# Kernel optimization log

Hardware: AMD Instinct MI355X
Metric: run time of the kernel (lower is better)

## Reference

```python
import jax, jax.numpy as jnp
from jax import lax
import numpy as np


def _lstm_layer(x, W_ih, W_hh, b_ih, b_hh):
    # x: (T, B, in_dim); gate order i, f, g, o (PyTorch convention)
    T, B, _ = x.shape
    H = W_hh.shape[1]
    # precompute input projections for all timesteps (one big GEMM)
    x_proj = jnp.einsum('tbi,gi->tbg', x, W_ih) + b_ih + b_hh  # (T, B, 4H)

    def step(carry, xt):
        h, c = carry
        gates = xt + h @ W_hh.T  # (B, 4H)
        i, f, g, o = jnp.split(gates, 4, axis=-1)
        c = jax.nn.sigmoid(f) * c + jax.nn.sigmoid(i) * jnp.tanh(g)
        h = jax.nn.sigmoid(o) * jnp.tanh(c)
        return (h, c), h

    h0 = jnp.zeros((B, H), dtype=x.dtype)
    c0 = jnp.zeros((B, H), dtype=x.dtype)
    (hT, cT), hs = lax.scan(step, (h0, c0), x_proj)
    return hs, hT, cT


def setup_inputs() -> dict:
    key = jax.random.key(0)
    ks = jax.random.split(key, 12)
    T, B, D_in, H, D_out = 1024, 64, 256, 512, 256
    s_in = 1.0 / np.sqrt(H)
    inp = {
        'x': jax.random.normal(ks[0], (T, B, D_in), jnp.float32),
        'W_ih0': jax.random.uniform(ks[1], (4 * H, D_in), jnp.float32, -s_in, s_in),
        'W_hh0': jax.random.uniform(ks[2], (4 * H, H), jnp.float32, -s_in, s_in),
        'b_ih0': jax.random.uniform(ks[3], (4 * H,), jnp.float32, -s_in, s_in),
        'b_hh0': jax.random.uniform(ks[4], (4 * H,), jnp.float32, -s_in, s_in),
        'W_ih1': jax.random.uniform(ks[5], (4 * H, H), jnp.float32, -s_in, s_in),
        'W_hh1': jax.random.uniform(ks[6], (4 * H, H), jnp.float32, -s_in, s_in),
        'b_ih1': jax.random.uniform(ks[7], (4 * H,), jnp.float32, -s_in, s_in),
        'b_hh1': jax.random.uniform(ks[8], (4 * H,), jnp.float32, -s_in, s_in),
        'W_out': jax.random.uniform(ks[9], (D_out, H), jnp.float32, -s_in, s_in),
        'b_out': jax.random.uniform(ks[10], (D_out,), jnp.float32, -s_in, s_in),
    }
    return inp


def reference(x, W_ih0, W_hh0, b_ih0, b_hh0, W_ih1, W_hh1, b_ih1, b_hh1, W_out, b_out):
    h1s, h1, c1 = _lstm_layer(x, W_ih0, W_hh0, b_ih0, b_hh0)
    h2s, h2, c2 = _lstm_layer(h1s, W_ih1, W_hh1, b_ih1, b_hh1)
    out = jnp.einsum('tbh,oh->tbo', h2s, W_out) + b_out  # (T, B, D_out)
    hn = jnp.stack([h1, h2], axis=0)  # (num_layers, B, H)
    cn = jnp.stack([c1, c2], axis=0)
    return (out, hn, cn)
```

## Files before the change

kernel.cpp:

```cpp
#include <hip/hip_runtime.h>

#define TT   1024
#define BB   64
#define DIN  256
#define HH   512
#define DOUT 256

#define NWG_L0  64
#define NWG_L1  128
#define NWG_OUT 8
#define NWG_TOT 200

typedef short bf16x8 __attribute__((ext_vector_type(8)));
typedef float f32x4  __attribute__((ext_vector_type(4)));
typedef unsigned u32x4 __attribute__((ext_vector_type(4)));

__device__ bf16x8 g_xf[TT * 2048];
__device__ bf16x8 g_h1f[8][4096];
__device__ bf16x8 g_h2f[8][4096];
__device__ bf16x8 g_h1z[4096];
__device__ bf16x8 g_h2z[4096];

__device__ unsigned g_flg[520 * 16];
__device__ unsigned g_iter;

__device__ __forceinline__ unsigned* FLG(int idx) { return &g_flg[idx * 16]; }

__device__ __forceinline__ u32x4 ldg_cv16(const void* p) {
    u32x4 r;
    asm volatile("global_load_dwordx4 %0, %1, off sc0 sc1"
                 : "=&v"(r) : "v"(p) : "memory");
    return r;
}
__device__ __forceinline__ void stg_cv16(void* p, u32x4 v) {
    asm volatile("global_store_dwordx4 %0, %1, off sc0 sc1" :: "v"(p), "v"(v) : "memory");
}
__device__ __forceinline__ void stg_cv_u32(void* p, unsigned v) {
    asm volatile("global_store_dword %0, %1, off sc0 sc1" :: "v"(p), "v"(v) : "memory");
}
__device__ __forceinline__ void wait_vm0(void) {
    asm volatile("s_waitcnt vmcnt(0)" ::: "memory");
}

__device__ __forceinline__ void waitpoll(const unsigned* p, unsigned tgt, int active, int tid) {
    for (;;) {
        unsigned v = 0xFFFFFFFFu;
        if (active)
            asm volatile("global_load_dword %0, %1, off sc0 sc1\n\t"
                         "s_waitcnt vmcnt(0)"
                         : "=&v"(v) : "v"(p) : "memory");
        if (__all(v >= tgt)) break;
        __builtin_amdgcn_s_sleep(1);
    }
    __syncthreads();
}

__device__ __forceinline__ float sigf(float v) { return 1.f / (1.f + __expf(-v)); }
__device__ __forceinline__ float tanh_fast(float v) { return 2.f / (1.f + __expf(-2.f * v)) - 1.f; }

__device__ __forceinline__ short f2bf(float f) {
    unsigned u = __builtin_bit_cast(unsigned, f);
    unsigned r = (u + 0x7FFFu + ((u >> 16) & 1u)) >> 16;
    return (short)r;
}

__device__ __forceinline__ bf16x8 pack8(float4 v0, float4 v1) {
    bf16x8 r;
    r[0] = f2bf(v0.x); r[1] = f2bf(v0.y); r[2] = f2bf(v0.z); r[3] = f2bf(v0.w);
    r[4] = f2bf(v1.x); r[5] = f2bf(v1.y); r[6] = f2bf(v1.z); r[7] = f2bf(v1.w);
    return r;
}

extern "C" __global__ void __launch_bounds__(256)
pack_x(const float* __restrict__ x) {
    const int t = blockIdx.x, tid = threadIdx.x;
    const float* xt = x + (size_t)t * BB * DIN;
    bf16x8* dst = g_xf + (size_t)t * 2048;
    #pragma unroll
    for (int u = 0; u < 8; ++u) {
        const int f = u * 256 + tid;
        const int lane_ = f & 63, ctks = f >> 6;
        const int ct = ctks & 3, ks = ctks >> 2;
        const int b  = ct * 16 + (lane_ & 15);
        const int kb = ks * 32 + (lane_ >> 4) * 8;
        const float4* s = (const float4*)(xt + b * DIN + kb);
        dst[f] = pack8(s[0], s[1]);
    }
}

__device__ void run_l0(int lwg, int tid,
                       const float* __restrict__ wih, const float* __restrict__ whh,
                       const float* __restrict__ bih, const float* __restrict__ bhh,
                       float* __restrict__ out, unsigned Q, bf16x8* sB, short* sH)
{
    constexpr int NCT = 2, NKSA = DIN / 32, NKS = NKSA + HH / 32;
    constexpr int NST = NKS * NCT / 4;
    constexpr int NCXR = NKSA * NCT / 4;

    const int lane = tid & 63, lo = lane & 15, hi = lane >> 4;
    const int w = tid >> 6;
    const int grp = lwg & 1, ub = lwg >> 1;
    const int ctbase = grp * 2;
    const int wv = ub * 4 + w, jbase = wv * 4;
    const int grow = (lo & 3) * HH + jbase + (lo >> 2);

    bf16x8 aF[NKS];
    #pragma unroll
    for (int ks = 0; ks < NKS; ++ks) {
        const float* wr = (ks < NKSA) ? wih + (size_t)grow * DIN + ks * 32 + hi * 8
                                      : whh + (size_t)grow * HH + (ks - NKSA) * 32 + hi * 8;
        const float4* p = (const float4*)wr;
        aF[ks] = pack8(p[0], p[1]);
    }
    f32x4 biasv;
    #pragma unroll
    for (int r = 0; r < 4; ++r)
        biasv[r] = bih[r * HH + jbase + hi] + bhh[r * HH + jbase + hi];

    const unsigned Qb = Q * 2048u;
    float cst[NCT] = {0.f, 0.f};

    for (int t = 0; t < TT; ++t) {
        {
            const unsigned* wp = g_flg; unsigned wt = 0; int wa = 0;
            const int bp = (t >= 8) && ((t & 3) == 0);
            if (w == 0) { if (lane < 32 && t >= 1) { wp = FLG(0 + grp * 32 + lane);
                                                     wt = Qb + t; wa = 1; } }
            else if (w == 1) { if (bp) {
                wp = FLG(192 + (grp * 2 + (lane >> 5)) * 32 + (lane & 31));
                wt = Qb + t - 4; wa = 1; } }
            else if (w == 2) { if (bp && lane < 32) {
                wp = FLG(320 + grp * 32 + lane); wt = Qb + t - 4; wa = 1; } }
            waitpoll(wp, wt, wa, tid);
        }

        const bf16x8* srcA = g_xf + (size_t)t * 2048;
        const bf16x8* srcB = (t == 0) ? g_h1z : g_h1f[(t - 1) & 7];

        u32x4 stg[NST];
        #pragma unroll
        for (int r = 0; r < NST; ++r) {
            const int ri = r * 4 + w, ks = ri / NCT, c = ri % NCT;
            if (r < NCXR) stg[r] = *(const u32x4*)&srcA[(ks * 4 + ctbase + c) * 64 + lane];
            else          stg[r] = ldg_cv16(&srcB[((ks - NKSA) * 4 + ctbase + c) * 64 + lane]);
        }
        wait_vm0();
        #pragma unroll
        for (int r = 0; r < NST; ++r)
            ((u32x4*)sB)[(r * 4 + w) * 64 + lane] = stg[r];
        __syncthreads();
        if (tid == 0) stg_cv_u32(FLG(320 + grp * 32 + ub), Qb + t);

        f32x4 acc[NCT] = {biasv, biasv};
        #pragma unroll
        for (int ks = 0; ks < NKS; ++ks)
            #pragma unroll
            for (int c = 0; c < NCT; ++c)
                acc[c] = __builtin_amdgcn_mfma_f32_16x16x32_bf16(
                    aF[ks], sB[(ks * NCT + c) * 64 + lane], acc[c], 0, 0, 0);

        #pragma unroll
        for (int c = 0; c < NCT; ++c) {
            const float gi = acc[c][0], gf = acc[c][1];
            const float gg = acc[c][2], go = acc[c][3];
            const float cn_ = sigf(gf) * cst[c] + sigf(gi) * tanh_fast(gg);
            const float hv  = sigf(go) * tanh_fast(cn_);
            cst[c] = cn_;
            sH[((c * 2 + (w >> 1)) * 16 + lo) * 8 + (w & 1) * 4 + hi] = f2bf(hv);
            if (t == TT - 1) {
                const int j = jbase + hi, b = (ctbase + c) * 16 + lo;
                const size_t base = (size_t)TT * BB * DOUT;
                out[base + (size_t)b * HH + j] = hv;
                out[base + (size_t)2 * BB * HH + (size_t)b * HH + j] = cn_;
            }
        }
        __syncthreads();

        u32x4* ringW = (u32x4*)g_h1f[t & 7];
        if (tid < 64) {
            const int c = tid >> 5, r = tid & 31, hi2 = r >> 4, lo2 = r & 15;
            const int f = ((ub >> 1) * 4 + ctbase + c) * 64 + ((ub & 1) * 2 + hi2) * 16 + lo2;
            stg_cv16(ringW + f, *(const u32x4*)&sH[((c * 2 + hi2) * 16 + lo2) * 8]);
        }
        wait_vm0();
        if (tid == 0) stg_cv_u32(FLG(0 + grp * 32 + ub), Qb + t + 1);
    }
}

__device__ void run_l1(int lwg, int tid,
                       const float* __restrict__ wih, const float* __restrict__ whh,
                       const float* __restrict__ bih, const float* __restrict__ bhh,
                       float* __restrict__ out, unsigned Q, bf16x8* sB, short* sH)
{
    constexpr int NKSA = HH / 32, NKS = 2 * NKSA;
    constexpr int NSTA = NKSA / 4, NSTB = NKSA / 4;

    const int lane = tid & 63, lo = lane & 15, hi = lane >> 4;
    const int w = tid >> 6;
    const int grp = lwg & 3, ub = lwg >> 2;
    const int ctbase = grp;
    const int wv = ub * 4 + w, jbase = wv * 4;
    const int grow = (lo & 3) * HH + jbase + (lo >> 2);

    bf16x8 aF[NKS];
    #pragma unroll
    for (int ks = 0; ks < NKS; ++ks) {
        const float* wr = (ks < NKSA) ? wih + (size_t)grow * HH + ks * 32 + hi * 8
                                      : whh + (size_t)grow * HH + (ks - NKSA) * 32 + hi * 8;
        const float4* p = (const float4*)wr;
        aF[ks] = pack8(p[0], p[1]);
    }
    f32x4 biasv;
    #pragma unroll
    for (int r = 0; r < 4; ++r)
        biasv[r] = bih[r * HH + jbase + hi] + bhh[r * HH + jbase + hi];

    const unsigned Qb = Q * 2048u;
    float cst = 0.f;

    {
        const unsigned* wp = g_flg; unsigned wt = 0; int wa = 0;
        if (w == 0 && lane < 32) { wp = FLG(0 + (grp >> 1) * 32 + lane); wt = Qb + 1; wa = 1; }
        waitpoll(wp, wt, wa, tid);
    }

    for (int t = 0; t < TT; ++t) {
        const bf16x8* srcA = g_h1f[t & 7];
        const bf16x8* srcB = (t == 0) ? g_h2z : g_h2f[(t - 1) & 7];

        u32x4 stgA[NSTA];
        #pragma unroll
        for (int r = 0; r < NSTA; ++r) {
            const int ks = r * 4 + w;
            stgA[r] = ldg_cv16(&srcA[(ks * 4 + ctbase) * 64 + lane]);
        }
        wait_vm0();
        #pragma unroll
        for (int r = 0; r < NSTA; ++r)
            ((u32x4*)sB)[(r * 4 + w) * 64 + lane] = stgA[r];
        __syncthreads();
        if (tid == 0) stg_cv_u32(FLG(192 + grp * 32 + ub), Qb + t + 1);

        {
            const unsigned* wp = g_flg; unsigned wt = 0; int wa = 0;
            if (w == 0 && lane < 32 && t >= 1) { wp = FLG(64 + grp * 32 + lane);
                                                 wt = Qb + t; wa = 1; }
            waitpoll(wp, wt, wa, tid);
        }

        u32x4 stgB[NSTB];
        #pragma unroll
        for (int r = 0; r < NSTB; ++r) {
            const int ks = r * 4 + w;
            stgB[r] = ldg_cv16(&srcB[(ks * 4 + ctbase) * 64 + lane]);
        }
        f32x4 acc = biasv;
        #pragma unroll
        for (int ks = 0; ks < NKSA; ++ks)
            acc = __builtin_amdgcn_mfma_f32_16x16x32_bf16(
                aF[ks], sB[ks * 64 + lane], acc, 0, 0, 0);
        wait_vm0();
        #pragma unroll
        for (int r = 0; r < NSTB; ++r)
            ((u32x4*)sB)[(NKSA + r * 4 + w) * 64 + lane] = stgB[r];
        __syncthreads();
        if (tid == 0) stg_cv_u32(FLG(384 + grp * 32 + ub), Qb + t);
        #pragma unroll
        for (int ks = NKSA; ks < NKS; ++ks)
            acc = __builtin_amdgcn_mfma_f32_16x16x32_bf16(
                aF[ks], sB[ks * 64 + lane], acc, 0, 0, 0);

        {
            const float gi = acc[0], gf = acc[1], gg = acc[2], go = acc[3];
            const float cn_ = sigf(gf) * cst + sigf(gi) * tanh_fast(gg);
            const float hv  = sigf(go) * tanh_fast(cn_);
            cst = cn_;
            sH[((w >> 1) * 16 + lo) * 8 + (w & 1) * 4 + hi] = f2bf(hv);
            if (t == TT - 1) {
                const int j = jbase + hi, b = ctbase * 16 + lo;
                const size_t base = (size_t)TT * BB * DOUT;
                out[base + (size_t)BB * HH + (size_t)b * HH + j] = hv;
                out[base + (size_t)3 * BB * HH + (size_t)b * HH + j] = cn_;
            }
        }
        __syncthreads();

        u32x4* ringW = (u32x4*)g_h2f[t & 7];
        if (tid < 32) {
            const int hi2 = tid >> 4, lo2 = tid & 15;
            const int f = ((ub >> 1) * 4 + ctbase) * 64 + ((ub & 1) * 2 + hi2) * 16 + lo2;
            stg_cv16(ringW + f, *(const u32x4*)&sH[(hi2 * 16 + lo2) * 8]);
        }
        wait_vm0();
        if (tid == 0) stg_cv_u32(FLG(64 + grp * 32 + ub), Qb + t + 1);

        if (t < TT - 1) {
            const unsigned* wp = g_flg; unsigned wt = 0; int wa = 0;
            const int bp = (t >= 7) && ((t & 3) == 3);
            if (w == 0) { if (lane < 32) { wp = FLG(0 + (grp >> 1) * 32 + lane);
                                           wt = Qb + t + 2; wa = 1; } }
            else if (w == 1) { if (bp) {
                if (lane < 32)      { wp = FLG(384 + grp * 32 + lane);
                                      wt = Qb + t - 3; wa = 1; }
                else if (lane < 36) { wp = FLG(512 + (grp >> 1) * 4 + (lane - 32));
                                      wt = Qb + t - 3; wa = 1; } } }
            waitpoll(wp, wt, wa, tid);
        }
    }
}

__device__ void run_out(int lwg, int tid,
                        const float* __restrict__ wout, const float* __restrict__ bout,
                        float* __restrict__ out, unsigned Q, bf16x8* sB)
{
    constexpr int NKS = HH / 32;
    constexpr int NST = 8;
    const int lane = tid & 63, lo = lane & 15, hi = lane >> 4;
    const int w = tid >> 6;
    const int cp = lwg & 1, ob = lwg >> 1;
    const int ctbase = cp * 2;
    const int obase = (ob * 4 + w) * 16;
    const unsigned Qb = Q * 2048u;

    bf16x8 aF[NKS];
    #pragma unroll
    for (int ks = 0; ks < NKS; ++ks) {
        const float4* p = (const float4*)(wout + (size_t)(obase + lo) * HH + ks * 32 + hi * 8);
        aF[ks] = pack8(p[0], p[1]);
    }
    f32x4 biasv;
    #pragma unroll
    for (int r = 0; r < 4; ++r) biasv[r] = bout[obase + hi * 4 + r];

    for (int t = 0; t < TT; ++t) {
        const unsigned* wp = g_flg; unsigned wt = 0; int wa = 0;
        if (w == 0) {
            wp = FLG(64 + (ctbase + (lane >> 5)) * 32 + (lane & 31));
            wt = Qb + t + 1; wa = 1;
        }
        waitpoll(wp, wt, wa, tid);

        const bf16x8* src = g_h2f[t & 7];
        u32x4 stg[NST];
        #pragma unroll
        for (int r = 0; r < NST; ++r) {
            const int ri = r * 4 + w;
            const int ks = ri >> 1, c = ri & 1;
            stg[r] = ldg_cv16(&src[(ks * 4 + ctbase + c) * 64 + lane]);
        }
        wait_vm0();
        #pragma unroll
        for (int r = 0; r < NST; ++r)
            ((u32x4*)sB)[(r * 4 + w) * 64 + lane] = stg[r];
        __syncthreads();
        if (tid == 0) stg_cv_u32(FLG(512 + cp * 4 + ob), Qb + t + 1);

        f32x4 acc[2] = {biasv, biasv};
        #pragma unroll
        for (int ks = 0; ks < NKS; ++ks)
            #pragma unroll
            for (int c = 0; c < 2; ++c)
                acc[c] = __builtin_amdgcn_mfma_f32_16x16x32_bf16(
                    aF[ks], sB[(ks * 2 + c) * 64 + lane], acc[c], 0, 0, 0);
        #pragma unroll
        for (int c = 0; c < 2; ++c)
            #pragma unroll
            for (int r = 0; r < 4; ++r) {
                const int b = (ctbase + c) * 16 + lo, o = obase + hi * 4 + r;
                out[(size_t)t * BB * DOUT + (size_t)b * DOUT + o] = acc[c][r];
            }
    }
}

extern "C" __global__ void __launch_bounds__(256, 1)
lstm2_fused(const float* __restrict__ x,
            const float* __restrict__ wih0, const float* __restrict__ whh0,
            const float* __restrict__ bih0, const float* __restrict__ bhh0,
            const float* __restrict__ wih1, const float* __restrict__ whh1,
            const float* __restrict__ bih1, const float* __restrict__ bhh1,
            const float* __restrict__ wout, const float* __restrict__ bout,
            float* __restrict__ out)
{
    __shared__ bf16x8 sB[3072];
    __shared__ __align__(16) short sH[2 * 2 * 16 * 8];

    const int tid = threadIdx.x, wg = blockIdx.x;
    const unsigned Q = __hip_atomic_load(&g_iter, __ATOMIC_RELAXED, __HIP_MEMORY_SCOPE_AGENT);

    if (wg < NWG_L0)
        run_l0(wg, tid, wih0, whh0, bih0, bhh0, out, Q, sB, sH);
    else if (wg < NWG_L0 + NWG_L1)
        run_l1(wg - NWG_L0, tid, wih1, whh1, bih1, bhh1, out, Q, sB, sH);
    else
        run_out(wg - NWG_L0 - NWG_L1, tid, wout, bout, out, Q, sB);

    if (wg == 0 && tid == 0)
        __hip_atomic_store(&g_iter, Q + 1, __ATOMIC_RELAXED, __HIP_MEMORY_SCOPE_AGENT);
}

extern "C" void kernel_launch(void* const* d_in, const int* in_sizes, int n_in,
                              void* d_out, int out_size, void* d_ws, size_t ws_size,
                              hipStream_t stream) {
    const float* x    = (const float*)d_in[0];
    const float* wih0 = (const float*)d_in[1];
    const float* whh0 = (const float*)d_in[2];
    const float* bih0 = (const float*)d_in[3];
    const float* bhh0 = (const float*)d_in[4];
    const float* wih1 = (const float*)d_in[5];
    const float* whh1 = (const float*)d_in[6];
    const float* bih1 = (const float*)d_in[7];
    const float* bhh1 = (const float*)d_in[8];
    const float* wout = (const float*)d_in[9];
    const float* bout = (const float*)d_in[10];
    float* out = (float*)d_out;

    hipLaunchKernelGGL(pack_x, dim3(TT), dim3(256), 0, stream, x);
    hipLaunchKernelGGL(lstm2_fused, dim3(NWG_TOT), dim3(256), 0, stream,
                       x, wih0, whh0, bih0, bhh0, wih1, whh1, bih1, bhh1,
                       wout, bout, out);
}
```

Measured before the change: 3.730 ms.

## Replace flag-based h-ring handoff with per-element tagged data polling

Hidden-state ring buffers now store each bf16 value together with a 16-bit iteration tag in a 32-bit word. Consumers poll the data itself until every tag matches, so producer-side flag stores, the LDS staging/sync before publishing, and separate readiness-flag waits are removed. This aims to shorten the per-timestep critical path of the recurrent dependency chain. In exchange it doubles the bytes moved per handoff and adds tag checks and repeated reloads while spinning.

Measured after the change: 5.194 ms. 1.39x slower.

```diff
diff --git a/kernel.cpp b/kernel.cpp
--- a/kernel.cpp
+++ b/kernel.cpp
@@ -16,10 +16,10 @@
 typedef unsigned u32x4 __attribute__((ext_vector_type(4)));
 
 __device__ bf16x8 g_xf[TT * 2048];
-__device__ bf16x8 g_h1f[8][4096];
-__device__ bf16x8 g_h2f[8][4096];
-__device__ bf16x8 g_h1z[4096];
-__device__ bf16x8 g_h2z[4096];
+
+#define SLOT_U32 (4 * 16 * 512)
+__device__ unsigned g_h1t[8][SLOT_U32];
+__device__ unsigned g_h2t[8][SLOT_U32];
 
 __device__ unsigned g_flg[520 * 16];
 __device__ unsigned g_iter;
@@ -31,9 +31,6 @@
     asm volatile("global_load_dwordx4 %0, %1, off sc0 sc1"
                  : "=&v"(r) : "v"(p) : "memory");
     return r;
-}
-__device__ __forceinline__ void stg_cv16(void* p, u32x4 v) {
-    asm volatile("global_store_dwordx4 %0, %1, off sc0 sc1" :: "v"(p), "v"(v) : "memory");
 }
 __device__ __forceinline__ void stg_cv_u32(void* p, unsigned v) {
     asm volatile("global_store_dword %0, %1, off sc0 sc1" :: "v"(p), "v"(v) : "memory");
@@ -55,6 +52,21 @@
     __syncthreads();
 }
 
+__device__ __forceinline__ int tagok(u32x4 a, u32x4 b, unsigned etag) {
+    return (int)((a[0] & 0xFFFFu) == etag) & (int)((a[1] & 0xFFFFu) == etag)
+         & (int)((a[2] & 0xFFFFu) == etag) & (int)((a[3] & 0xFFFFu) == etag)
+         & (int)((b[0] & 0xFFFFu) == etag) & (int)((b[1] & 0xFFFFu) == etag)
+         & (int)((b[2] & 0xFFFFu) == etag) & (int)((b[3] & 0xFFFFu) == etag);
+}
+__device__ __forceinline__ u32x4 untag(u32x4 a, u32x4 b) {
+    u32x4 p;
+    p[0] = (a[0] >> 16) | (a[1] & 0xFFFF0000u);
+    p[1] = (a[2] >> 16) | (a[3] & 0xFFFF0000u);
+    p[2] = (b[0] >> 16) | (b[1] & 0xFFFF0000u);
+    p[3] = (b[2] >> 16) | (b[3] & 0xFFFF0000u);
+    return p;
+}
+
 __device__ __forceinline__ float sigf(float v) { return 1.f / (1.f + __expf(-v)); }
 __device__ __forceinline__ float tanh_fast(float v) { return 2.f / (1.f + __expf(-2.f * v)) - 1.f; }
 
@@ -69,6 +81,10 @@
     r[0] = f2bf(v0.x); r[1] = f2bf(v0.y); r[2] = f2bf(v0.z); r[3] = f2bf(v0.w);
     r[4] = f2bf(v1.x); r[5] = f2bf(v1.y); r[6] = f2bf(v1.z); r[7] = f2bf(v1.w);
     return r;
+}
+
+__device__ __forceinline__ int pidx_of(int j, int b) {
+    return ((j >> 5) * 4 + (b >> 4)) * 512 + (((j >> 3) & 3) * 16 + (b & 15)) * 8 + (j & 7);
 }
 
 extern "C" __global__ void __launch_bounds__(256)
@@ -91,17 +107,14 @@
 __device__ void run_l0(int lwg, int tid,
                        const float* __restrict__ wih, const float* __restrict__ whh,
                        const float* __restrict__ bih, const float* __restrict__ bhh,
-                       float* __restrict__ out, unsigned Q, bf16x8* sB, short* sH)
+                       float* __restrict__ out, unsigned Q, bf16x8* sB)
 {
-    constexpr int NCT = 2, NKSA = DIN / 32, NKS = NKSA + HH / 32;
-    constexpr int NST = NKS * NCT / 4;
-    constexpr int NCXR = NKSA * NCT / 4;
-
+    constexpr int NKSA = 8, NKS = 24;
     const int lane = tid & 63, lo = lane & 15, hi = lane >> 4;
     const int w = tid >> 6;
     const int grp = lwg & 1, ub = lwg >> 1;
     const int ctbase = grp * 2;
-    const int wv = ub * 4 + w, jbase = wv * 4;
+    const int jbase = (ub * 4 + w) * 4;
     const int grow = (lo & 3) * HH + jbase + (lo >> 2);
 
     bf16x8 aF[NKS];
@@ -118,88 +131,102 @@
         biasv[r] = bih[r * HH + jbase + hi] + bhh[r * HH + jbase + hi];
 
     const unsigned Qb = Q * 2048u;
-    float cst[NCT] = {0.f, 0.f};
+    float cst[2] = {0.f, 0.f};
 
     for (int t = 0; t < TT; ++t) {
-        {
-            const unsigned* wp = g_flg; unsigned wt = 0; int wa = 0;
-            const int bp = (t >= 8) && ((t & 3) == 0);
-            if (w == 0) { if (lane < 32 && t >= 1) { wp = FLG(0 + grp * 32 + lane);
-                                                     wt = Qb + t; wa = 1; } }
-            else if (w == 1) { if (bp) {
-                wp = FLG(192 + (grp * 2 + (lane >> 5)) * 32 + (lane & 31));
-                wt = Qb + t - 4; wa = 1; } }
-            else if (w == 2) { if (bp && lane < 32) {
-                wp = FLG(320 + grp * 32 + lane); wt = Qb + t - 4; wa = 1; } }
-            waitpoll(wp, wt, wa, tid);
-        }
-
-        const bf16x8* srcA = g_xf + (size_t)t * 2048;
-        const bf16x8* srcB = (t == 0) ? g_h1z : g_h1f[(t - 1) & 7];
-
-        u32x4 stg[NST];
-        #pragma unroll
-        for (int r = 0; r < NST; ++r) {
-            const int ri = r * 4 + w, ks = ri / NCT, c = ri % NCT;
-            if (r < NCXR) stg[r] = *(const u32x4*)&srcA[(ks * 4 + ctbase + c) * 64 + lane];
-            else          stg[r] = ldg_cv16(&srcB[((ks - NKSA) * 4 + ctbase + c) * 64 + lane]);
-        }
-        wait_vm0();
-        #pragma unroll
-        for (int r = 0; r < NST; ++r)
-            ((u32x4*)sB)[(r * 4 + w) * 64 + lane] = stg[r];
+        __syncthreads();
+
+        u32x4 sa[4];
+        #pragma unroll
+        for (int r = 0; r < 4; ++r) {
+            const int ri = r * 4 + w, ks = ri >> 1, c = ri & 1;
+            sa[r] = *(const u32x4*)&g_xf[(size_t)t * 2048 + (ks * 4 + ctbase + c) * 64 + lane];
+        }
+        #pragma unroll
+        for (int r = 0; r < 4; ++r)
+            ((u32x4*)sB)[(r * 4 + w) * 64 + lane] = sa[r];
+
+        if (t > 0) {
+            const unsigned etag = (Qb + t) & 0xFFFFu;
+            const unsigned* slot = g_h1t[(t - 1) & 7];
+            u32x4 da[8], db[8];
+            for (;;) {
+                #pragma unroll
+                for (int r = 0; r < 8; ++r) {
+                    const int ri = r * 4 + w, ks = ri >> 1, c = ri & 1;
+                    const unsigned* p = slot + (ks * 4 + ctbase + c) * 512 + lane * 8;
+                    da[r] = ldg_cv16(p); db[r] = ldg_cv16(p + 4);
+                }
+                wait_vm0();
+                int ok = 1;
+                #pragma unroll
+                for (int r = 0; r < 8; ++r) ok &= tagok(da[r], db[r], etag);
+                if (__all(ok)) break;
+                __builtin_amdgcn_s_sleep(1);
+            }
+            #pragma unroll
+            for (int r = 0; r < 8; ++r)
+                ((u32x4*)sB)[(16 + r * 4 + w) * 64 + lane] = untag(da[r], db[r]);
+        }
         __syncthreads();
         if (tid == 0) stg_cv_u32(FLG(320 + grp * 32 + ub), Qb + t);
 
-        f32x4 acc[NCT] = {biasv, biasv};
-        #pragma unroll
-        for (int ks = 0; ks < NKS; ++ks)
-            #pragma unroll
-            for (int c = 0; c < NCT; ++c)
+        if (((t & 3) == 0) && t >= 8) {
+            const unsigned* wp = g_flg; unsigned wt = 0; int wa = 0;
+            if (w == 1) { wp = FLG(192 + (2 * grp + (lane >> 5)) * 32 + (lane & 31));
+                          wt = Qb + t - 4; wa = 1; }
+            else if (w == 2 && lane < 32) { wp = FLG(320 + grp * 32 + lane);
+                                            wt = Qb + t - 4; wa = 1; }
+            waitpoll(wp, wt, wa, tid);
+        }
+
+        f32x4 acc[2] = {biasv, biasv};
+        #pragma unroll
+        for (int ks = 0; ks < NKSA; ++ks)
+            #pragma unroll
+            for (int c = 0; c < 2; ++c)
                 acc[c] = __builtin_amdgcn_mfma_f32_16x16x32_bf16(
-                    aF[ks], sB[(ks * NCT + c) * 64 + lane], acc[c], 0, 0, 0);
-
-        #pragma unroll
-        for (int c = 0; c < NCT; ++c) {
+                    aF[ks], sB[(ks * 2 + c) * 64 + lane], acc[c], 0, 0, 0);
+        if (t > 0) {
+            #pragma unroll
+            for (int ks = NKSA; ks < NKS; ++ks)
+                #pragma unroll
+                for (int c = 0; c < 2; ++c)
+                    acc[c] = __builtin_amdgcn_mfma_f32_16x16x32_bf16(
+                        aF[ks], sB[(ks * 2 + c) * 64 + lane], acc[c], 0, 0, 0);
+        }
+
+        const unsigned ptag = (Qb + t + 1) & 0xFFFFu;
+        unsigned* slotW = g_h1t[t & 7];
+        #pragma unroll
+        for (int c = 0; c < 2; ++c) {
             const float gi = acc[c][0], gf = acc[c][1];
             const float gg = acc[c][2], go = acc[c][3];
             const float cn_ = sigf(gf) * cst[c] + sigf(gi) * tanh_fast(gg);
             const float hv  = sigf(go) * tanh_fast(cn_);
             cst[c] = cn_;
-            sH[((c * 2 + (w >> 1)) * 16 + lo) * 8 + (w & 1) * 4 + hi] = f2bf(hv);
+            const int j = jbase + hi, b = (ctbase + c) * 16 + lo;
+            stg_cv_u32(slotW + pidx_of(j, b),
+                       ((unsigned)(unsigned short)f2bf(hv) << 16) | ptag);
             if (t == TT - 1) {
-                const int j = jbase + hi, b = (ctbase + c) * 16 + lo;
                 const size_t base = (size_t)TT * BB * DOUT;
                 out[base + (size_t)b * HH + j] = hv;
                 out[base + (size_t)2 * BB * HH + (size_t)b * HH + j] = cn_;
             }
         }
-        __syncthreads();
-
-        u32x4* ringW = (u32x4*)g_h1f[t & 7];
-        if (tid < 64) {
-            const int c = tid >> 5, r = tid & 31, hi2 = r >> 4, lo2 = r & 15;
-            const int f = ((ub >> 1) * 4 + ctbase + c) * 64 + ((ub & 1) * 2 + hi2) * 16 + lo2;
-            stg_cv16(ringW + f, *(const u32x4*)&sH[((c * 2 + hi2) * 16 + lo2) * 8]);
-        }
-        wait_vm0();
-        if (tid == 0) stg_cv_u32(FLG(0 + grp * 32 + ub), Qb + t + 1);
     }
 }
 
 __device__ void run_l1(int lwg, int tid,
                        const float* __restrict__ wih, const float* __restrict__ whh,
                        const float* __restrict__ bih, const float* __restrict__ bhh,
-                       float* __restrict__ out, unsigned Q, bf16x8* sB, short* sH)
+                       float* __restrict__ out, unsigned Q, bf16x8* sB)
 {
-    constexpr int NKSA = HH / 32, NKS = 2 * NKSA;
-    constexpr int NSTA = NKSA / 4, NSTB = NKSA / 4;
-
+    constexpr int NKSA = 16, NKS = 32;
     const int lane = tid & 63, lo = lane & 15, hi = lane >> 4;
     const int w = tid >> 6;
     const int grp = lwg & 3, ub = lwg >> 2;
-    const int ctbase = grp;
-    const int wv = ub * 4 + w, jbase = wv * 4;
+    const int jbase = (ub * 4 + w) * 4;
     const int grow = (lo & 3) * HH + jbase + (lo >> 2);
 
     bf16x8 aF[NKS];
@@ -218,93 +245,98 @@
     const unsigned Qb = Q * 2048u;
     float cst = 0.f;
 
-    {
-        const unsigned* wp = g_flg; unsigned wt = 0; int wa = 0;
-        if (w == 0 && lane < 32) { wp = FLG(0 + (grp >> 1) * 32 + lane); wt = Qb + 1; wa = 1; }
-        waitpoll(wp, wt, wa, tid);
-    }
-
     for (int t = 0; t < TT; ++t) {
-        const bf16x8* srcA = g_h1f[t & 7];
-        const bf16x8* srcB = (t == 0) ? g_h2z : g_h2f[(t - 1) & 7];
-
-        u32x4 stgA[NSTA];
-        #pragma unroll
-        for (int r = 0; r < NSTA; ++r) {
-            const int ks = r * 4 + w;
-            stgA[r] = ldg_cv16(&srcA[(ks * 4 + ctbase) * 64 + lane]);
-        }
-        wait_vm0();
-        #pragma unroll
-        for (int r = 0; r < NSTA; ++r)
-            ((u32x4*)sB)[(r * 4 + w) * 64 + lane] = stgA[r];
+        {
+            const unsigned etag = (Qb + t + 1) & 0xFFFFu;
+            const unsigned* slot = g_h1t[t & 7];
+            u32x4 da[4], db[4];
+            for (;;) {
+                #pragma unroll
+                for (int r = 0; r < 4; ++r) {
+                    const unsigned* p = slot + ((r * 4 + w) * 4 + grp) * 512 + lane * 8;
+                    da[r] = ldg_cv16(p); db[r] = ldg_cv16(p + 4);
+                }
+                wait_vm0();
+                int ok = 1;
+                #pragma unroll
+                for (int r = 0; r < 4; ++r) ok &= tagok(da[r], db[r], etag);
+                if (__all(ok)) break;
+                __builtin_amdgcn_s_sleep(1);
+            }
+            #pragma unroll
+            for (int r = 0; r < 4; ++r)
+                ((u32x4*)sB)[(r * 4 + w) * 64 + lane] = untag(da[r], db[r]);
+        }
         __syncthreads();
         if (tid == 0) stg_cv_u32(FLG(192 + grp * 32 + ub), Qb + t + 1);
 
-        {
+        f32x4 acc = biasv;
+        if (t > 0) {
+            const unsigned etag = (Qb + t) & 0xFFFFu;
+            const unsigned* slot = g_h2t[(t - 1) & 7];
+            u32x4 da[4], db[4];
+            #pragma unroll
+            for (int r = 0; r < 4; ++r) {
+                const unsigned* p = slot + ((r * 4 + w) * 4 + grp) * 512 + lane * 8;
+                da[r] = ldg_cv16(p); db[r] = ldg_cv16(p + 4);
+            }
+            #pragma unroll
+            for (int ks = 0; ks < NKSA; ++ks)
+                acc = __builtin_amdgcn_mfma_f32_16x16x32_bf16(
+                    aF[ks], sB[ks * 64 + lane], acc, 0, 0, 0);
+            for (;;) {
+                wait_vm0();
+                int ok = 1;
+                #pragma unroll
+                for (int r = 0; r < 4; ++r) ok &= tagok(da[r], db[r], etag);
+                if (__all(ok)) break;
+                __builtin_amdgcn_s_sleep(1);
+                #pragma unroll
+                for (int r = 0; r < 4; ++r) {
+                    const unsigned* p = slot + ((r * 4 + w) * 4 + grp) * 512 + lane * 8;
+                    da[r] = ldg_cv16(p); db[r] = ldg_cv16(p + 4);
+                }
+            }
+            #pragma unroll
+            for (int r = 0; r < 4; ++r)
+                ((u32x4*)sB)[(16 + r * 4 + w) * 64 + lane] = untag(da[r], db[r]);
+            __syncthreads();
+            if (tid == 0) stg_cv_u32(FLG(384 + grp * 32 + ub), Qb + t);
+            #pragma unroll
+            for (int ks = NKSA; ks < NKS; ++ks)
+                acc = __builtin_amdgcn_mfma_f32_16x16x32_bf16(
+                    aF[ks], sB[ks * 64 + lane], acc, 0, 0, 0);
+        } else {
+            #pragma unroll
+            for (int ks = 0; ks < NKSA; ++ks)
+                acc = __builtin_amdgcn_mfma_f32_16x16x32_bf16(
+                    aF[ks], sB[ks * 64 + lane], acc, 0, 0, 0);
+            __syncthreads();
+            if (tid == 0) stg_cv_u32(FLG(384 + grp * 32 + ub), Qb);
+        }
+
+        if (((t & 3) == 0) && t >= 8) {
             const unsigned* wp = g_flg; unsigned wt = 0; int wa = 0;
-            if (w == 0 && lane < 32 && t >= 1) { wp = FLG(64 + grp * 32 + lane);
-                                                 wt = Qb + t; wa = 1; }
+            if (w == 1) {
+                if (lane < 32)      { wp = FLG(384 + grp * 32 + lane); wt = Qb + t - 4; wa = 1; }
+                else if (lane < 36) { wp = FLG(512 + (grp >> 1) * 4 + (lane - 32));
+                                      wt = Qb + t - 4; wa = 1; }
+            }
             waitpoll(wp, wt, wa, tid);
         }
 
-        u32x4 stgB[NSTB];
-        #pragma unroll
-        for (int r = 0; r < NSTB; ++r) {
-            const int ks = r * 4 + w;
-            stgB[r] = ldg_cv16(&srcB[(ks * 4 + ctbase) * 64 + lane]);
-        }
-        f32x4 acc = biasv;
-        #pragma unroll
-        for (int ks = 0; ks < NKSA; ++ks)
-            acc = __builtin_amdgcn_mfma_f32_16x16x32_bf16(
-                aF[ks], sB[ks * 64 + lane], acc, 0, 0, 0);
-        wait_vm0();
-        #pragma unroll
-        for (int r = 0; r < NSTB; ++r)
-            ((u32x4*)sB)[(NKSA + r * 4 + w) * 64 + lane] = stgB[r];
-        __syncthreads();
-        if (tid == 0) stg_cv_u32(FLG(384 + grp * 32 + ub), Qb + t);
-        #pragma unroll
-        for (int ks = NKSA; ks < NKS; ++ks)
-            acc = __builtin_amdgcn_mfma_f32_16x16x32_bf16(
-                aF[ks], sB[ks * 64 + lane], acc, 0, 0, 0);
-
-        {
-            const float gi = acc[0], gf = acc[1], gg = acc[2], go = acc[3];
-            const float cn_ = sigf(gf) * cst + sigf(gi) * tanh_fast(gg);
-            const float hv  = sigf(go) * tanh_fast(cn_);
-            cst = cn_;
-            sH[((w >> 1) * 16 + lo) * 8 + (w & 1) * 4 + hi] = f2bf(hv);
-            if (t == TT - 1) {
-                const int j = jbase + hi, b = ctbase * 16 + lo;
-                const size_t base = (size_t)TT * BB * DOUT;
-                out[base + (size_t)BB * HH + (size_t)b * HH + j] = hv;
-                out[base + (size_t)3 * BB * HH + (size_t)b * HH + j] = cn_;
-            }
-        }
-        __syncthreads();
-
-        u32x4* ringW = (u32x4*)g_h2f[t & 7];
-        if (tid < 32) {
-            const int hi2 = tid >> 4, lo2 = tid & 15;
-            const int f = ((ub >> 1) * 4 + ctbase) * 64 + ((ub & 1) * 2 + hi2) * 16 + lo2;
-            stg_cv16(ringW + f, *(const u32x4*)&sH[(hi2 * 16 + lo2) * 8]);
-        }
-        wait_vm0();
-        if (tid == 0) stg_cv_u32(FLG(64 + grp * 32 + ub), Qb + t + 1);
-
-        if (t < TT - 1) {
-            const unsigned* wp = g_flg; unsigned wt = 0; int wa = 0;
-            const int bp = (t >= 7) && ((t & 3) == 3);
-            if (w == 0) { if (lane < 32) { wp = FLG(0 + (grp >> 1) * 32 + lane);
-                                           wt = Qb + t + 2; wa = 1; } }
-            else if (w == 1) { if (bp) {
-                if (lane < 32)      { wp = FLG(384 + grp * 32 + lane);
-                                      wt = Qb + t - 3; wa = 1; }
-                else if (lane < 36) { wp = FLG(512 + (grp >> 1) * 4 + (lane - 32));
-                                      wt = Qb + t - 3; wa = 1; } } }
-            waitpoll(wp, wt, wa, tid);
+        const float gi = acc[0], gf = acc[1], gg = acc[2], go = acc[3];
+        const float cn_ = sigf(gf) * cst + sigf(gi) * tanh_fast(gg);
+        const float hv  = sigf(go) * tanh_fast(cn_);
+        cst = cn_;
+        const unsigned ptag = (Qb + t + 1) & 0xFFFFu;
+        const int j = jbase + hi, b = grp * 16 + lo;
+        stg_cv_u32(g_h2t[t & 7] + pidx_of(j, b),
+                   ((unsigned)(unsigned short)f2bf(hv) << 16) | ptag);
+        if (t == TT - 1) {
+            const size_t base = (size_t)TT * BB * DOUT;
+            out[base + (size_t)BB * HH + (size_t)b * HH + j] = hv;
+            out[base + (size_t)3 * BB * HH + (size_t)b * HH + j] = cn_;
         }
     }
 }
@@ -314,7 +346,6 @@
                         float* __restrict__ out, unsigned Q, bf16x8* sB)
 {
     constexpr int NKS = HH / 32;
-    constexpr int NST = 8;
     const int lane = tid & 63, lo = lane & 15, hi = lane >> 4;
     const int w = tid >> 6;
     const int cp = lwg & 1, ob = lwg >> 1;
@@ -333,25 +364,29 @@
     for (int r = 0; r < 4; ++r) biasv[r] = bout[obase + hi * 4 + r];
 
     for (int t = 0; t < TT; ++t) {
-        const unsigned* wp = g_flg; unsigned wt = 0; int wa = 0;
-        if (w == 0) {
-            wp = FLG(64 + (ctbase + (lane >> 5)) * 32 + (lane & 31));
-            wt = Qb + t + 1; wa = 1;
-        }
-        waitpoll(wp, wt, wa, tid);
-
-        const bf16x8* src = g_h2f[t & 7];
-        u32x4 stg[NST];
-        #pragma unroll
-        for (int r = 0; r < NST; ++r) {
-            const int ri = r * 4 + w;
-            const int ks = ri >> 1, c = ri & 1;
-            stg[r] = ldg_cv16(&src[(ks * 4 + ctbase + c) * 64 + lane]);
-        }
-        wait_vm0();
-        #pragma unroll
-        for (int r = 0; r < NST; ++r)
-            ((u32x4*)sB)[(r * 4 + w) * 64 + lane] = stg[r];
+        __syncthreads();
+        {
+            const unsigned etag = (Qb + t + 1) & 0xFFFFu;
+            const unsigned* slot = g_h2t[t & 7];
+            u32x4 da[8], db[8];
+            for (;;) {
+                #pragma unroll
+                for (int r = 0; r < 8; ++r) {
+                    const int ri = r * 4 + w, ks = ri >> 1, c = ri & 1;
+                    const unsigned* p = slot + (ks * 4 + ctbase + c) * 512 + lane * 8;
+                    da[r] = ldg_cv16(p); db[r] = ldg_cv16(p + 4);
+                }
+                wait_vm0();
+                int ok = 1;
+                #pragma unroll
+                for (int r = 0; r < 8; ++r) ok &= tagok(da[r], db[r], etag);
+                if (__all(ok)) break;
+                __builtin_amdgcn_s_sleep(1);
+            }
+            #pragma unroll
+            for (int r = 0; r < 8; ++r)
+                ((u32x4*)sB)[(r * 4 + w) * 64 + lane] = untag(da[r], db[r]);
+        }
         __syncthreads();
         if (tid == 0) stg_cv_u32(FLG(512 + cp * 4 + ob), Qb + t + 1);
 
@@ -382,15 +417,14 @@
             float* __restrict__ out)
 {
     __shared__ bf16x8 sB[3072];
-    __shared__ __align__(16) short sH[2 * 2 * 16 * 8];
 
     const int tid = threadIdx.x, wg = blockIdx.x;
     const unsigned Q = __hip_atomic_load(&g_iter, __ATOMIC_RELAXED, __HIP_MEMORY_SCOPE_AGENT);
 
     if (wg < NWG_L0)
-        run_l0(wg, tid, wih0, whh0, bih0, bhh0, out, Q, sB, sH);
+        run_l0(wg, tid, wih0, whh0, bih0, bhh0, out, Q, sB);
     else if (wg < NWG_L0 + NWG_L1)
-        run_l1(wg - NWG_L0, tid, wih1, whh1, bih1, bhh1, out, Q, sB, sH);
+        run_l1(wg - NWG_L0, tid, wih1, whh1, bih1, bhh1, out, Q, sB);
     else
         run_out(wg - NWG_L0 - NWG_L1, tid, wout, bout, out, Q, sB);
 
```

## Halve workgroup count with 8-wave workgroups to cut cross-WG flag polling

Applied to the files above, without the earlier changes.

Doubles the threads per workgroup to 512 (8 waves) and halves the number of workgroups per stage (layer0 32, layer1 64, output 4). Each workgroup now owns 32 hidden units instead of 16, so h-chunk ring writes and flag waits involve half as many producers. The change also drops the zero-initialised h buffers by skipping the recurrent MFMA at t=0, and restructures layer1 so all waits happen at the top of each step. The cost is more per-workgroup synchronisation over larger barriers and fewer CUs in use, which lowers parallelism per step.

Measured after the change: 3.996 ms. +7.1%, slower.

```diff
diff --git a/kernel.cpp b/kernel.cpp
--- a/kernel.cpp
+++ b/kernel.cpp
@@ -6,10 +6,10 @@
 #define HH   512
 #define DOUT 256
 
-#define NWG_L0  64
-#define NWG_L1  128
-#define NWG_OUT 8
-#define NWG_TOT 200
+#define NWG_L0  32
+#define NWG_L1  64
+#define NWG_OUT 4
+#define NWG_TOT 100
 
 typedef short bf16x8 __attribute__((ext_vector_type(8)));
 typedef float f32x4  __attribute__((ext_vector_type(4)));
@@ -18,10 +18,8 @@
 __device__ bf16x8 g_xf[TT * 2048];
 __device__ bf16x8 g_h1f[8][4096];
 __device__ bf16x8 g_h2f[8][4096];
-__device__ bf16x8 g_h1z[4096];
-__device__ bf16x8 g_h2z[4096];
-
-__device__ unsigned g_flg[520 * 16];
+
+__device__ unsigned g_flg[260 * 16];
 __device__ unsigned g_iter;
 
 __device__ __forceinline__ unsigned* FLG(int idx) { return &g_flg[idx * 16]; }
@@ -93,15 +91,12 @@
                        const float* __restrict__ bih, const float* __restrict__ bhh,
                        float* __restrict__ out, unsigned Q, bf16x8* sB, short* sH)
 {
-    constexpr int NCT = 2, NKSA = DIN / 32, NKS = NKSA + HH / 32;
-    constexpr int NST = NKS * NCT / 4;
-    constexpr int NCXR = NKSA * NCT / 4;
-
+    constexpr int NKSA = 8, NKS = 24;
     const int lane = tid & 63, lo = lane & 15, hi = lane >> 4;
     const int w = tid >> 6;
     const int grp = lwg & 1, ub = lwg >> 1;
     const int ctbase = grp * 2;
-    const int wv = ub * 4 + w, jbase = wv * 4;
+    const int jbase = ub * 32 + w * 4;
     const int grow = (lo & 3) * HH + jbase + (lo >> 2);
 
     bf16x8 aF[NKS];
@@ -118,55 +113,69 @@
         biasv[r] = bih[r * HH + jbase + hi] + bhh[r * HH + jbase + hi];
 
     const unsigned Qb = Q * 2048u;
-    float cst[NCT] = {0.f, 0.f};
+    float cst[2] = {0.f, 0.f};
 
     for (int t = 0; t < TT; ++t) {
         {
             const unsigned* wp = g_flg; unsigned wt = 0; int wa = 0;
             const int bp = (t >= 8) && ((t & 3) == 0);
-            if (w == 0) { if (lane < 32 && t >= 1) { wp = FLG(0 + grp * 32 + lane);
+            if (w == 0) { if (lane < 16 && t >= 1) { wp = FLG(0 + grp * 16 + lane);
                                                      wt = Qb + t; wa = 1; } }
-            else if (w == 1) { if (bp) {
-                wp = FLG(192 + (grp * 2 + (lane >> 5)) * 32 + (lane & 31));
-                wt = Qb + t - 4; wa = 1; } }
-            else if (w == 2) { if (bp && lane < 32) {
-                wp = FLG(320 + grp * 32 + lane); wt = Qb + t - 4; wa = 1; } }
+            else if (w == 1 && bp) {
+                if (lane < 32)      { wp = FLG(96 + (2 * grp + (lane >> 4)) * 16 + (lane & 15));
+                                      wt = Qb + t - 4; wa = 1; }
+                else if (lane < 48) { wp = FLG(160 + grp * 16 + (lane - 32));
+                                      wt = Qb + t - 4; wa = 1; }
+            }
             waitpoll(wp, wt, wa, tid);
         }
 
         const bf16x8* srcA = g_xf + (size_t)t * 2048;
-        const bf16x8* srcB = (t == 0) ? g_h1z : g_h1f[(t - 1) & 7];
-
-        u32x4 stg[NST];
-        #pragma unroll
-        for (int r = 0; r < NST; ++r) {
-            const int ri = r * 4 + w, ks = ri / NCT, c = ri % NCT;
-            if (r < NCXR) stg[r] = *(const u32x4*)&srcA[(ks * 4 + ctbase + c) * 64 + lane];
-            else          stg[r] = ldg_cv16(&srcB[((ks - NKSA) * 4 + ctbase + c) * 64 + lane]);
+        const bf16x8* srcB = g_h1f[(t - 1) & 7];
+        u32x4 stg[6];
+        #pragma unroll
+        for (int r = 0; r < 6; ++r) {
+            const int ri = r * 8 + w;
+            if (ri < 16) {
+                const int ks = ri >> 1, c = ri & 1;
+                stg[r] = *(const u32x4*)&srcA[(ks * 4 + ctbase + c) * 64 + lane];
+            } else if (t > 0) {
+                const int ks = (ri - 16) >> 1, c = (ri - 16) & 1;
+                stg[r] = ldg_cv16(&srcB[(ks * 4 + ctbase + c) * 64 + lane]);
+            }
         }
         wait_vm0();
         #pragma unroll
-        for (int r = 0; r < NST; ++r)
-            ((u32x4*)sB)[(r * 4 + w) * 64 + lane] = stg[r];
+        for (int r = 0; r < 6; ++r)
+            ((u32x4*)sB)[(r * 8 + w) * 64 + lane] = stg[r];
         __syncthreads();
-        if (tid == 0) stg_cv_u32(FLG(320 + grp * 32 + ub), Qb + t);
-
-        f32x4 acc[NCT] = {biasv, biasv};
-        #pragma unroll
-        for (int ks = 0; ks < NKS; ++ks)
-            #pragma unroll
-            for (int c = 0; c < NCT; ++c)
+        if (tid == 0) stg_cv_u32(FLG(160 + grp * 16 + ub), Qb + t);
+
+        f32x4 acc[2] = {biasv, biasv};
+        #pragma unroll
+        for (int ks = 0; ks < NKSA; ++ks)
+            #pragma unroll
+            for (int c = 0; c < 2; ++c)
                 acc[c] = __builtin_amdgcn_mfma_f32_16x16x32_bf16(
-                    aF[ks], sB[(ks * NCT + c) * 64 + lane], acc[c], 0, 0, 0);
-
-        #pragma unroll
-        for (int c = 0; c < NCT; ++c) {
+                    aF[ks], sB[(ks * 2 + c) * 64 + lane], acc[c], 0, 0, 0);
+        if (t > 0) {
+            #pragma unroll
+            for (int ks = NKSA; ks < NKS; ++ks)
+                #pragma unroll
+                for (int c = 0; c < 2; ++c)
+                    acc[c] = __builtin_amdgcn_mfma_f32_16x16x32_bf16(
+                        aF[ks], sB[(ks * 2 + c) * 64 + lane], acc[c], 0, 0, 0);
+        }
+
+        #pragma unroll
+        for (int c = 0; c < 2; ++c) {
             const float gi = acc[c][0], gf = acc[c][1];
             const float gg = acc[c][2], go = acc[c][3];
             const float cn_ = sigf(gf) * cst[c] + sigf(gi) * tanh_fast(gg);
             const float hv  = sigf(go) * tanh_fast(cn_);
             cst[c] = cn_;
-            sH[((c * 2 + (w >> 1)) * 16 + lo) * 8 + (w & 1) * 4 + hi] = f2bf(hv);
+            const int jp = w * 4 + hi;
+            sH[(c * 64 + (jp >> 3) * 16 + lo) * 8 + (jp & 7)] = f2bf(hv);
             if (t == TT - 1) {
                 const int j = jbase + hi, b = (ctbase + c) * 16 + lo;
                 const size_t base = (size_t)TT * BB * DOUT;
@@ -178,12 +187,13 @@
 
         u32x4* ringW = (u32x4*)g_h1f[t & 7];
         if (tid < 64) {
-            const int c = tid >> 5, r = tid & 31, hi2 = r >> 4, lo2 = r & 15;
-            const int f = ((ub >> 1) * 4 + ctbase + c) * 64 + ((ub & 1) * 2 + hi2) * 16 + lo2;
-            stg_cv16(ringW + f, *(const u32x4*)&sH[((c * 2 + hi2) * 16 + lo2) * 8]);
+            #pragma unroll
+            for (int c = 0; c < 2; ++c)
+                stg_cv16(ringW + (ub * 4 + ctbase + c) * 64 + tid,
+                         *(const u32x4*)&sH[(c * 64 + tid) * 8]);
         }
         wait_vm0();
-        if (tid == 0) stg_cv_u32(FLG(0 + grp * 32 + ub), Qb + t + 1);
+        if (tid == 0) stg_cv_u32(FLG(0 + grp * 16 + ub), Qb + t + 1);
     }
 }
 
@@ -192,14 +202,11 @@
                        const float* __restrict__ bih, const float* __restrict__ bhh,
                        float* __restrict__ out, unsigned Q, bf16x8* sB, short* sH)
 {
-    constexpr int NKSA = HH / 32, NKS = 2 * NKSA;
-    constexpr int NSTA = NKSA / 4, NSTB = NKSA / 4;
-
+    constexpr int NKSA = 16, NKS = 32;
     const int lane = tid & 63, lo = lane & 15, hi = lane >> 4;
     const int w = tid >> 6;
     const int grp = lwg & 3, ub = lwg >> 2;
-    const int ctbase = grp;
-    const int wv = ub * 4 + w, jbase = wv * 4;
+    const int jbase = ub * 32 + w * 4;
     const int grow = (lo & 3) * HH + jbase + (lo >> 2);
 
     bf16x8 aF[NKS];
@@ -218,66 +225,82 @@
     const unsigned Qb = Q * 2048u;
     float cst = 0.f;
 
-    {
-        const unsigned* wp = g_flg; unsigned wt = 0; int wa = 0;
-        if (w == 0 && lane < 32) { wp = FLG(0 + (grp >> 1) * 32 + lane); wt = Qb + 1; wa = 1; }
-        waitpoll(wp, wt, wa, tid);
-    }
-
     for (int t = 0; t < TT; ++t) {
-        const bf16x8* srcA = g_h1f[t & 7];
-        const bf16x8* srcB = (t == 0) ? g_h2z : g_h2f[(t - 1) & 7];
-
-        u32x4 stgA[NSTA];
-        #pragma unroll
-        for (int r = 0; r < NSTA; ++r) {
-            const int ks = r * 4 + w;
-            stgA[r] = ldg_cv16(&srcA[(ks * 4 + ctbase) * 64 + lane]);
-        }
-        wait_vm0();
-        #pragma unroll
-        for (int r = 0; r < NSTA; ++r)
-            ((u32x4*)sB)[(r * 4 + w) * 64 + lane] = stgA[r];
-        __syncthreads();
-        if (tid == 0) stg_cv_u32(FLG(192 + grp * 32 + ub), Qb + t + 1);
-
         {
             const unsigned* wp = g_flg; unsigned wt = 0; int wa = 0;
-            if (w == 0 && lane < 32 && t >= 1) { wp = FLG(64 + grp * 32 + lane);
+            const int bp = (t >= 8) && ((t & 3) == 0);
+            if (w == 0) { if (lane < 16) { wp = FLG(0 + (grp >> 1) * 16 + lane);
+                                           wt = Qb + t + 1; wa = 1; } }
+            else if (w == 1 && bp) {
+                if (lane < 16)      { wp = FLG(192 + grp * 16 + lane);
+                                      wt = Qb + t - 4; wa = 1; }
+                else if (lane < 18) { wp = FLG(256 + 2 * (grp >> 1) + (lane - 16));
+                                      wt = Qb + t - 4; wa = 1; }
+            }
+            waitpoll(wp, wt, wa, tid);
+        }
+
+        const bf16x8* srcA = g_h1f[t & 7];
+        u32x4 sa[2];
+        #pragma unroll
+        for (int r = 0; r < 2; ++r) {
+            const int ks = r * 8 + w;
+            sa[r] = ldg_cv16(&srcA[(ks * 4 + grp) * 64 + lane]);
+        }
+        wait_vm0();
+        #pragma unroll
+        for (int r = 0; r < 2; ++r)
+            ((u32x4*)sB)[(r * 8 + w) * 64 + lane] = sa[r];
+        __syncthreads();
+        if (tid == 0) stg_cv_u32(FLG(96 + grp * 16 + ub), Qb + t + 1);
+
+        {
+            const unsigned* wp = g_flg; unsigned wt = 0; int wa = 0;
+            if (w == 0 && lane < 16 && t >= 1) { wp = FLG(32 + grp * 16 + lane);
                                                  wt = Qb + t; wa = 1; }
             waitpoll(wp, wt, wa, tid);
         }
 
-        u32x4 stgB[NSTB];
-        #pragma unroll
-        for (int r = 0; r < NSTB; ++r) {
-            const int ks = r * 4 + w;
-            stgB[r] = ldg_cv16(&srcB[(ks * 4 + ctbase) * 64 + lane]);
-        }
         f32x4 acc = biasv;
-        #pragma unroll
-        for (int ks = 0; ks < NKSA; ++ks)
-            acc = __builtin_amdgcn_mfma_f32_16x16x32_bf16(
-                aF[ks], sB[ks * 64 + lane], acc, 0, 0, 0);
-        wait_vm0();
-        #pragma unroll
-        for (int r = 0; r < NSTB; ++r)
-            ((u32x4*)sB)[(NKSA + r * 4 + w) * 64 + lane] = stgB[r];
-        __syncthreads();
-        if (tid == 0) stg_cv_u32(FLG(384 + grp * 32 + ub), Qb + t);
-        #pragma unroll
-        for (int ks = NKSA; ks < NKS; ++ks)
-            acc = __builtin_amdgcn_mfma_f32_16x16x32_bf16(
-                aF[ks], sB[ks * 64 + lane], acc, 0, 0, 0);
+        if (t > 0) {
+            const bf16x8* srcB = g_h2f[(t - 1) & 7];
+            u32x4 sb[2];
+            #pragma unroll
+            for (int r = 0; r < 2; ++r) {
+                const int ks = r * 8 + w;
+                sb[r] = ldg_cv16(&srcB[(ks * 4 + grp) * 64 + lane]);
+            }
+            #pragma unroll
+            for (int ks = 0; ks < NKSA; ++ks)
+                acc = __builtin_amdgcn_mfma_f32_16x16x32_bf16(
+                    aF[ks], sB[ks * 64 + lane], acc, 0, 0, 0);
+            wait_vm0();
+            #pragma unroll
+            for (int r = 0; r < 2; ++r)
+                ((u32x4*)sB)[(16 + r * 8 + w) * 64 + lane] = sb[r];
+            __syncthreads();
+            if (tid == 0) stg_cv_u32(FLG(192 + grp * 16 + ub), Qb + t);
+            #pragma unroll
+            for (int ks = NKSA; ks < NKS; ++ks)
+                acc = __builtin_amdgcn_mfma_f32_16x16x32_bf16(
+                    aF[ks], sB[ks * 64 + lane], acc, 0, 0, 0);
+        } else {
+            #pragma unroll
+            for (int ks = 0; ks < NKSA; ++ks)
+                acc = __builtin_amdgcn_mfma_f32_16x16x32_bf16(
+                    aF[ks], sB[ks * 64 + lane], acc, 0, 0, 0);
+            if (tid == 0) stg_cv_u32(FLG(192 + grp * 16 + ub), Qb);
+        }
 
         {
             const float gi = acc[0], gf = acc[1], gg = acc[2], go = acc[3];
             const float cn_ = sigf(gf) * cst + sigf(gi) * tanh_fast(gg);
             const float hv  = sigf(go) * tanh_fast(cn_);
             cst = cn_;
-            sH[((w >> 1) * 16 + lo) * 8 + (w & 1) * 4 + hi] = f2bf(hv);
+            const int jp = w * 4 + hi;
+            sH[((jp >> 3) * 16 + lo) * 8 + (jp & 7)] = f2bf(hv);
             if (t == TT - 1) {
-                const int j = jbase + hi, b = ctbase * 16 + lo;
+                const int j = jbase + hi, b = grp * 16 + lo;
                 const size_t base = (size_t)TT * BB * DOUT;
                 out[base + (size_t)BB * HH + (size_t)b * HH + j] = hv;
                 out[base + (size_t)3 * BB * HH + (size_t)b * HH + j] = cn_;
@@ -286,40 +309,23 @@
         __syncthreads();
 
         u32x4* ringW = (u32x4*)g_h2f[t & 7];
-        if (tid < 32) {
-            const int hi2 = tid >> 4, lo2 = tid & 15;
-            const int f = ((ub >> 1) * 4 + ctbase) * 64 + ((ub & 1) * 2 + hi2) * 16 + lo2;
-            stg_cv16(ringW + f, *(const u32x4*)&sH[(hi2 * 16 + lo2) * 8]);
-        }
+        if (tid < 64)
+            stg_cv16(ringW + (ub * 4 + grp) * 64 + tid, *(const u32x4*)&sH[tid * 8]);
         wait_vm0();
-        if (tid == 0) stg_cv_u32(FLG(64 + grp * 32 + ub), Qb + t + 1);
-
-        if (t < TT - 1) {
-            const unsigned* wp = g_flg; unsigned wt = 0; int wa = 0;
-            const int bp = (t >= 7) && ((t & 3) == 3);
-            if (w == 0) { if (lane < 32) { wp = FLG(0 + (grp >> 1) * 32 + lane);
-                                           wt = Qb + t + 2; wa = 1; } }
-            else if (w == 1) { if (bp) {
-                if (lane < 32)      { wp = FLG(384 + grp * 32 + lane);
-                                      wt = Qb + t - 3; wa = 1; }
-                else if (lane < 36) { wp = FLG(512 + (grp >> 1) * 4 + (lane - 32));
-                                      wt = Qb + t - 3; wa = 1; } } }
-            waitpoll(wp, wt, wa, tid);
-        }
-    }
-}
-
-__device__ void run_out(int lwg, int tid,
+        if (tid == 0) stg_cv_u32(FLG(32 + grp * 16 + ub), Qb + t + 1);
+    }
+}
+
+__device__ void run_out(int o, int tid,
                         const float* __restrict__ wout, const float* __restrict__ bout,
                         float* __restrict__ out, unsigned Q, bf16x8* sB)
 {
     constexpr int NKS = HH / 32;
-    constexpr int NST = 8;
     const int lane = tid & 63, lo = lane & 15, hi = lane >> 4;
     const int w = tid >> 6;
-    const int cp = lwg & 1, ob = lwg >> 1;
+    const int cp = o >> 1, ob = o & 1;
     const int ctbase = cp * 2;
-    const int obase = (ob * 4 + w) * 16;
+    const int obase = ob * 128 + w * 16;
     const unsigned Qb = Q * 2048u;
 
     bf16x8 aF[NKS];
@@ -333,27 +339,27 @@
     for (int r = 0; r < 4; ++r) biasv[r] = bout[obase + hi * 4 + r];
 
     for (int t = 0; t < TT; ++t) {
-        const unsigned* wp = g_flg; unsigned wt = 0; int wa = 0;
-        if (w == 0) {
-            wp = FLG(64 + (ctbase + (lane >> 5)) * 32 + (lane & 31));
-            wt = Qb + t + 1; wa = 1;
-        }
-        waitpoll(wp, wt, wa, tid);
-
+        {
+            const unsigned* wp = g_flg; unsigned wt = 0; int wa = 0;
+            if (w == 0 && lane < 32) {
+                wp = FLG(32 + (ctbase + (lane >> 4)) * 16 + (lane & 15));
+                wt = Qb + t + 1; wa = 1;
+            }
+            waitpoll(wp, wt, wa, tid);
+        }
         const bf16x8* src = g_h2f[t & 7];
-        u32x4 stg[NST];
-        #pragma unroll
-        for (int r = 0; r < NST; ++r) {
-            const int ri = r * 4 + w;
-            const int ks = ri >> 1, c = ri & 1;
+        u32x4 stg[4];
+        #pragma unroll
+        for (int r = 0; r < 4; ++r) {
+            const int ri = r * 8 + w, ks = ri >> 1, c = ri & 1;
             stg[r] = ldg_cv16(&src[(ks * 4 + ctbase + c) * 64 + lane]);
         }
         wait_vm0();
         #pragma unroll
-        for (int r = 0; r < NST; ++r)
-            ((u32x4*)sB)[(r * 4 + w) * 64 + lane] = stg[r];
+        for (int r = 0; r < 4; ++r)
+            ((u32x4*)sB)[(r * 8 + w) * 64 + lane] = stg[r];
         __syncthreads();
-        if (tid == 0) stg_cv_u32(FLG(512 + cp * 4 + ob), Qb + t + 1);
+        if (tid == 0) stg_cv_u32(FLG(256 + o), Qb + t + 1);
 
         f32x4 acc[2] = {biasv, biasv};
         #pragma unroll
@@ -366,13 +372,13 @@
         for (int c = 0; c < 2; ++c)
             #pragma unroll
             for (int r = 0; r < 4; ++r) {
-                const int b = (ctbase + c) * 16 + lo, o = obase + hi * 4 + r;
-                out[(size_t)t * BB * DOUT + (size_t)b * DOUT + o] = acc[c][r];
-            }
-    }
-}
-
-extern "C" __global__ void __launch_bounds__(256, 1)
+                const int b = (ctbase + c) * 16 + lo, oo = obase + hi * 4 + r;
+                out[(size_t)t * BB * DOUT + (size_t)b * DOUT + oo] = acc[c][r];
+            }
+    }
+}
+
+extern "C" __global__ void __launch_bounds__(512, 1)
 lstm2_fused(const float* __restrict__ x,
             const float* __restrict__ wih0, const float* __restrict__ whh0,
             const float* __restrict__ bih0, const float* __restrict__ bhh0,
@@ -382,7 +388,7 @@
             float* __restrict__ out)
 {
     __shared__ bf16x8 sB[3072];
-    __shared__ __align__(16) short sH[2 * 2 * 16 * 8];
+    __shared__ __align__(16) short sH[2 * 64 * 8];
 
     const int tid = threadIdx.x, wg = blockIdx.x;
     const unsigned Q = __hip_atomic_load(&g_iter, __ATOMIC_RELAXED, __HIP_MEMORY_SCOPE_AGENT);
@@ -415,7 +421,7 @@
     float* out = (float*)d_out;
 
     hipLaunchKernelGGL(pack_x, dim3(TT), dim3(256), 0, stream, x);
-    hipLaunchKernelGGL(lstm2_fused, dim3(NWG_TOT), dim3(256), 0, stream,
+    hipLaunchKernelGGL(lstm2_fused, dim3(NWG_TOT), dim3(512), 0, stream,
                        x, wih0, whh0, bih0, bhh0, wih1, whh1, bih1, bhh1,
                        wout, bout, out);
 }
```
